# Optimization experiments

Measured on AMD Instinct MI355X. Metric: run time of the kernel, lower is better.

Reference implementation:

```python
import jax, jax.numpy as jnp
import numpy as np
from jax import lax

HUMAN_SIZE = 54
NUM_ACTIONS = 1
INPUT_SIZE = HUMAN_SIZE + NUM_ACTIONS  # 55, one_hot=True
RNN_SIZE = 1024
SOURCE_SEQ_LEN = 50
TARGET_SEQ_LEN = 25
BATCH = 1024


def setup_inputs() -> dict:
    key = jax.random.key(0)
    ks = jax.random.split(key, 8)
    s = 1.0 / np.sqrt(RNN_SIZE)
    return {
        "encoder_inputs": jax.random.normal(ks[0], (BATCH, SOURCE_SEQ_LEN, INPUT_SIZE), jnp.float32),
        "decoder_inputs": jax.random.normal(ks[1], (BATCH, TARGET_SEQ_LEN, INPUT_SIZE), jnp.float32),
        "W_ih": jax.random.uniform(ks[2], (3 * RNN_SIZE, INPUT_SIZE), jnp.float32, -s, s),
        "W_hh": jax.random.uniform(ks[3], (3 * RNN_SIZE, RNN_SIZE), jnp.float32, -s, s),
        "b_ih": jax.random.uniform(ks[4], (3 * RNN_SIZE,), jnp.float32, -s, s),
        "b_hh": jax.random.uniform(ks[5], (3 * RNN_SIZE,), jnp.float32, -s, s),
        "fc_w": jax.random.uniform(ks[6], (INPUT_SIZE, RNN_SIZE), jnp.float32, -s, s),
        "fc_b": jax.random.uniform(ks[7], (INPUT_SIZE,), jnp.float32, -s, s),
    }


def _gru_step(h, x, W_ih, W_hh, b_ih, b_hh):
    # torch.nn.GRUCell math
    gi = x @ W_ih.T + b_ih            # [B, 3H]
    gh = h @ W_hh.T + b_hh            # [B, 3H]
    i_r, i_z, i_n = jnp.split(gi, 3, axis=-1)
    h_r, h_z, h_n = jnp.split(gh, 3, axis=-1)
    r = jax.nn.sigmoid(i_r + h_r)
    z = jax.nn.sigmoid(i_z + h_z)
    n = jnp.tanh(i_n + r * h_n)
    return (1.0 - z) * n + z * h


def reference(encoder_inputs, decoder_inputs, W_ih, W_hh, b_ih, b_hh, fc_w, fc_b):
    B = encoder_inputs.shape[0]
    H = W_hh.shape[1]
    state0 = jnp.zeros((B, H), dtype=encoder_inputs.dtype)

    # Encoder: first source_seq_len-1 frames, time-major scan (dropout p=0 -> identity)
    enc_tm = jnp.swapaxes(encoder_inputs[:, : SOURCE_SEQ_LEN - 1], 0, 1)  # [S-1, B, In]

    def enc_step(h, x):
        return _gru_step(h, x, W_ih, W_hh, b_ih, b_hh), None

    state, _ = lax.scan(enc_step, state0, enc_tm)

    def dec_step(carry, _):
        h, inp = carry
        inp = lax.stop_gradient(inp)  # inp.detach()
        h = _gru_step(h, inp, W_ih, W_hh, b_ih, b_hh)
        out = inp + h @ fc_w.T + fc_b  # residual add
        return (h, out), out

    (_, _), outs = lax.scan(dec_step, (state, decoder_inputs[:, 0]), None, length=TARGET_SEQ_LEN)
    return jnp.swapaxes(outs, 0, 1)  # [B, T, In]
```

## Files before the change

### kernel.cpp

```cpp
#include <hip/hip_runtime.h>


typedef unsigned short ushort_t;
typedef __bf16 bf16x8 __attribute__((ext_vector_type(8)));
typedef float f32x4 __attribute__((ext_vector_type(4)));
typedef unsigned int u32x4 __attribute__((ext_vector_type(4)));

#define MFMA(a, b, c) __builtin_amdgcn_mfma_f32_16x16x32_bf16(a, b, c, 0, 0, 0)

static __device__ __forceinline__ ushort_t f2bf(float f) {
  union { float f; unsigned u; } x; x.f = f;
  unsigned r = x.u + 0x7fffu + ((x.u >> 16) & 1u);
  return (ushort_t)(r >> 16);
}
static __device__ __forceinline__ float sigmf(float x) { return 1.f / (1.f + __expf(-x)); }
static __device__ __forceinline__ float tanhf_(float x) { return 1.f - 2.f / (__expf(2.f * x) + 1.f); }

static __device__ __forceinline__ __amdgpu_buffer_rsrc_t mkrsrc(const void* p) {
  return __builtin_amdgcn_make_buffer_rsrc(const_cast<void*>(p), (short)0, -1, 0x00020000);
}
#if __has_builtin(__builtin_amdgcn_raw_buffer_load_b128)
static __device__ __forceinline__ bf16x8 ldb(__amdgpu_buffer_rsrc_t r, int voff) {
  u32x4 v = __builtin_amdgcn_raw_buffer_load_b128(r, voff, 0, 1);
  union { u32x4 u; bf16x8 b; } x; x.u = v; return x.b;
}
static __device__ __forceinline__ bf16x8 ldbc(__amdgpu_buffer_rsrc_t r, int voff) {
  u32x4 v = __builtin_amdgcn_raw_buffer_load_b128(r, voff, 0, 0);
  union { u32x4 u; bf16x8 b; } x; x.u = v; return x.b;
}
#else
static __device__ __forceinline__ bf16x8 ldb(__amdgpu_buffer_rsrc_t r, int voff) {
  union { unsigned u[4]; bf16x8 b; } x;
  x.u[0] = __builtin_amdgcn_raw_buffer_load_b32(r, voff, 0, 1);
  x.u[1] = __builtin_amdgcn_raw_buffer_load_b32(r, voff + 4, 0, 1);
  x.u[2] = __builtin_amdgcn_raw_buffer_load_b32(r, voff + 8, 0, 1);
  x.u[3] = __builtin_amdgcn_raw_buffer_load_b32(r, voff + 12, 0, 1);
  return x.b;
}
static __device__ __forceinline__ bf16x8 ldbc(__amdgpu_buffer_rsrc_t r, int voff) {
  union { unsigned u[4]; bf16x8 b; } x;
  x.u[0] = __builtin_amdgcn_raw_buffer_load_b32(r, voff, 0, 0);
  x.u[1] = __builtin_amdgcn_raw_buffer_load_b32(r, voff + 4, 0, 0);
  x.u[2] = __builtin_amdgcn_raw_buffer_load_b32(r, voff + 8, 0, 0);
  x.u[3] = __builtin_amdgcn_raw_buffer_load_b32(r, voff + 12, 0, 0);
  return x.b;
}
#endif

__global__ __launch_bounds__(512, 2)
void seq2seq_xcd(const float* __restrict__ enc, const float* __restrict__ dec,
                 const float* __restrict__ Wih, const float* __restrict__ Whh,
                 const float* __restrict__ b_ih, const float* __restrict__ b_hh,
                 const float* __restrict__ fcw, const float* __restrict__ fcb,
                 float* __restrict__ outp,
                 ushort_t* __restrict__ xg, ushort_t* __restrict__ hA,
                 ushort_t* __restrict__ innA, ushort_t* __restrict__ nG,
                 ushort_t* __restrict__ fcG, unsigned* cnt) {
  __shared__ ushort_t WrzL[65536];
  __shared__ ushort_t WiL[6144];
  __shared__ float scratchF[4096];
  __shared__ unsigned sgs;

  const int tid = threadIdx.x;
  const int w = tid >> 6, l = tid & 63;
  const int fr = l & 15, fq4 = l >> 4;

  if (tid == 0) {
    unsigned x;
    asm volatile("s_getreg_b32 %0, hwreg(HW_REG_XCC_ID, 0, 8)" : "=s"(x));
    x &= 7u;
    unsigned s = atomicAdd(&cnt[x * 64], 1u);
    sgs = (x << 8) | s;
  }
  __syncthreads();
  const int g = sgs >> 8, slot = sgs & 255;
  const bool isFC = (slot >= 24);

  unsigned* arrp = cnt + (8 + g) * 64;
  auto fcpp = [&](int td) { return cnt + (48 + g * 25 + td) * 64; };

  ushort_t* hbase = hA + (size_t)g * 262144;
  auto hb = [&](int i) { return hbase + (size_t)i * 131072; };
  ushort_t* xgg = xg + (size_t)g * 49 * 8192;
  auto inng = [&](int i) { return innA + (size_t)(g * 2 + i) * 8192; };
  ushort_t* nGp = nG + (size_t)(g * 32 + slot) * 32768;
  ushort_t* fcGg = fcG + (size_t)g * 65536;

  for (int i = tid; i < 65536; i += 512) {
    int j = i & 7, ln = (i >> 3) & 63, jf = (i >> 9) & 1, gt = (i >> 10) & 1, kt = i >> 11;
    int col = gt * 1024 + slot * 32 + jf * 16 + (ln & 15);
    int k = kt * 32 + (ln >> 4) * 8 + j;
    WrzL[i] = f2bf(Whh[(size_t)col * 1024 + k]);
  }
  for (int i = tid; i < 6144; i += 512) {
    int j = i & 7, ln = (i >> 3) & 63, jf = (i >> 9) & 1, rem = i >> 10;
    int gt = rem % 3, kt = rem / 3;
    int col = gt * 1024 + slot * 32 + jf * 16 + (ln & 15);
    int k = kt * 32 + (ln >> 4) * 8 + j;
    WiL[i] = (k < 55) ? f2bf(Wih[(size_t)col * 55 + k]) : (ushort_t)0;
  }
  for (int i = tid; i < 32768; i += 512) {
    int j = i & 7, ln = (i >> 3) & 63, jf = (i >> 9) & 1, kt = i >> 10;
    int col = 2048 + slot * 32 + jf * 16 + (ln & 15);
    int k = kt * 32 + (ln >> 4) * 8 + j;
    nGp[i] = f2bf(Whh[(size_t)col * 1024 + k]);
  }
#pragma unroll
  for (int rep = 0; rep < 2; ++rep) {
    int t = slot + rep * 32;
    if (t < 49) {
      ushort_t* xp = xgg + (size_t)t * 8192;
      for (int i = tid; i < 8192; i += 512) {
        int sub = i & 7, row = (i >> 3) & 127, kc = i >> 10;
        int c = kc * 8 + sub;
        xp[i] = (c < 55) ? f2bf(enc[((size_t)(g * 128 + row) * 50 + t) * 55 + c]) : (ushort_t)0;
      }
    }
  }
  if (slot < 4) {
    ushort_t* ip = inng(0);
    for (int i = slot * 2048 + tid; i < (slot + 1) * 2048; i += 512) {
      int sub = i & 7, row = (i >> 3) & 127, kc = i >> 10;
      int c = kc * 8 + sub;
      ip[i] = (c < 55) ? f2bf(dec[(size_t)(g * 128 + row) * 1375 + c]) : (ushort_t)0;
    }
  }
  if (isFC) {
    for (int i = (slot - 24) * 8192 + tid; i < (slot - 23) * 8192; i += 512) {
      int j = i & 7, ln = (i >> 3) & 63, jf = (i >> 9) & 3, kt = i >> 11;
      int c = jf * 16 + (ln & 15);
      int k = kt * 32 + (ln >> 4) * 8 + j;
      fcGg[i] = (c < 55) ? f2bf(fcw[(size_t)c * 1024 + k]) : (ushort_t)0;
    }
  }

  float brz[2], bzz[2], bin[2], bhn[2];
#pragma unroll
  for (int jf = 0; jf < 2; ++jf) {
    int col = slot * 32 + jf * 16 + fr;
    brz[jf] = b_ih[col] + b_hh[col];
    bzz[jf] = b_ih[1024 + col] + b_hh[1024 + col];
    bin[jf] = b_ih[2048 + col];
    bhn[jf] = b_hh[2048 + col];
  }
  const int Rfc = (slot - 24) * 16;
  const int jfF = w & 3;
  const int colF = jfF * 16 + fr;
  float fcbF = 0.f, inp[4] = {0.f, 0.f, 0.f, 0.f};
  if (isFC && w < 4) {
    fcbF = (colF < 55) ? fcb[colF] : 0.f;
#pragma unroll
    for (int v = 0; v < 4; ++v)
      inp[v] = (colF < 55) ? dec[(size_t)(g * 128 + Rfc + fq4 * 4 + v) * 1375 + colF] : 0.f;
  }
  f32x4 hreg[4];
#pragma unroll
  for (int i = 0; i < 4; ++i) hreg[i] = (f32x4){0.f, 0.f, 0.f, 0.f};

  auto arrive = [&](unsigned k) {
    (void)k;
    __syncthreads();
    if (tid == 0) atomicAdd(arrp, 1u);
  };
  auto wait_rel = [&](unsigned k) {
    if (tid == 0) {
      while (__hip_atomic_load(arrp, __ATOMIC_RELAXED, __HIP_MEMORY_SCOPE_AGENT) < 32u * k)
        __builtin_amdgcn_s_sleep(1);
    }
    __syncthreads();
  };
  auto fc_wait = [&](int td) {
    if (tid == 0) {
      while (__hip_atomic_load(fcpp(td), __ATOMIC_RELAXED, __HIP_MEMORY_SCOPE_AGENT) < 8u)
        __builtin_amdgcn_s_sleep(1);
    }
    __syncthreads();
  };

  f32x4 av[12], nx[4];

  auto xpart = [&](const ushort_t* xp) {
    __amdgpu_buffer_rsrc_t rx = mkrsrc(xp);
    const int R = w * 32;
#pragma unroll
    for (int kt = 0; kt < 2; ++kt) {
      bf16x8 a0 = ldb(rx, ((kt * 4 + fq4) * 128 + R + fr) * 16);
      bf16x8 a1 = ldb(rx, ((kt * 4 + fq4) * 128 + R + 16 + fr) * 16);
      const ushort_t* bl = WiL + kt * 3072 + l * 8;
#pragma unroll
      for (int jf = 0; jf < 2; ++jf) {
        bf16x8 br = *(const bf16x8*)(bl + jf * 512);
        bf16x8 bz = *(const bf16x8*)(bl + 1024 + jf * 512);
        bf16x8 bn = *(const bf16x8*)(bl + 2048 + jf * 512);
        av[jf] = MFMA(a0, br, av[jf]);
        av[2 + jf] = MFMA(a1, br, av[2 + jf]);
        av[4 + jf] = MFMA(a0, bz, av[4 + jf]);
        av[6 + jf] = MFMA(a1, bz, av[6 + jf]);
        nx[jf] = MFMA(a0, bn, nx[jf]);
        nx[2 + jf] = MFMA(a1, bn, nx[2 + jf]);
      }
    }
  };

  auto hpart = [&](const ushort_t* hbp) {
    __amdgpu_buffer_rsrc_t r = mkrsrc(hbp);
    __amdgpu_buffer_rsrc_t rn = mkrsrc(nGp);
    const int kh = w >> 2, R = (w & 3) * 32;
    bf16x8 A0[4], A1[4];
    bf16x8 NG[4][2];
#pragma unroll
    for (int i = 0; i < 4; ++i) {
      int kt = kh * 16 + i;
      A0[i] = ldb(r, ((kt * 4 + fq4) * 128 + R + fr) * 16);
      A1[i] = ldb(r, ((kt * 4 + fq4) * 128 + R + 16 + fr) * 16);
      NG[i][0] = ldbc(rn, kt * 2048 + l * 16);
      NG[i][1] = ldbc(rn, kt * 2048 + 1024 + l * 16);
    }
    const ushort_t* bl0 = WrzL + (kh * 16) * 2048 + l * 8;
    bf16x8 br0 = *(const bf16x8*)(bl0);
    bf16x8 br1 = *(const bf16x8*)(bl0 + 512);
    bf16x8 bz0 = *(const bf16x8*)(bl0 + 1024);
    bf16x8 bz1 = *(const bf16x8*)(bl0 + 1536);
#pragma unroll
    for (int i = 0; i < 16; ++i) {
      int kt = kh * 16 + i;
      bf16x8 a0 = A0[i & 3], a1 = A1[i & 3];
      bf16x8 n0 = NG[i & 3][0], n1 = NG[i & 3][1];
      bf16x8 cr0 = br0, cr1 = br1, cz0 = bz0, cz1 = bz1;
      if (i < 15) {
        const ushort_t* bln = WrzL + (kt + 1) * 2048 + l * 8;
        br0 = *(const bf16x8*)(bln);
        br1 = *(const bf16x8*)(bln + 512);
        bz0 = *(const bf16x8*)(bln + 1024);
        bz1 = *(const bf16x8*)(bln + 1536);
      }
      if (i < 12) {
        int kp = kt + 4;
        A0[i & 3] = ldb(r, ((kp * 4 + fq4) * 128 + R + fr) * 16);
        A1[i & 3] = ldb(r, ((kp * 4 + fq4) * 128 + R + 16 + fr) * 16);
        NG[i & 3][0] = ldbc(rn, kp * 2048 + l * 16);
        NG[i & 3][1] = ldbc(rn, kp * 2048 + 1024 + l * 16);
      }
      av[0] = MFMA(a0, cr0, av[0]);
      av[2] = MFMA(a1, cr0, av[2]);
      av[1] = MFMA(a0, cr1, av[1]);
      av[3] = MFMA(a1, cr1, av[3]);
      av[4] = MFMA(a0, cz0, av[4]);
      av[6] = MFMA(a1, cz0, av[6]);
      av[5] = MFMA(a0, cz1, av[5]);
      av[7] = MFMA(a1, cz1, av[7]);
      av[8] = MFMA(a0, n0, av[8]);
      av[10] = MFMA(a1, n0, av[10]);
      av[9] = MFMA(a0, n1, av[9]);
      av[11] = MFMA(a1, n1, av[11]);
    }
  };

  auto kreduce = [&]() {
#pragma unroll
    for (int rd = 0; rd < 3; ++rd) {
      if (w >= 4) {
        float* sp = scratchF + ((w - 4) * 64 + l) * 4;
#pragma unroll
        for (int r = 0; r < 4; ++r)
          *(f32x4*)(sp + r * 1024) = av[rd * 4 + r];
      }
      __syncthreads();
      if (w < 4) {
        const float* sp = scratchF + (w * 64 + l) * 4;
#pragma unroll
        for (int r = 0; r < 4; ++r)
          av[rd * 4 + r] += *(const f32x4*)(sp + r * 1024);
      }
      __syncthreads();
    }
  };

  auto fcdo = [&](const ushort_t* hbp, int td, bool wr, ushort_t* innW) {
    __amdgpu_buffer_rsrc_t r = mkrsrc(hbp);
    __amdgpu_buffer_rsrc_t rf = mkrsrc(fcGg);
    const int kh = w >> 2;
    f32x4 fa = (f32x4){0.f, 0.f, 0.f, 0.f};
    bf16x8 Af[4], Bf[4];
#pragma unroll
    for (int i = 0; i < 4; ++i) {
      int kt = kh * 16 + i;
      Af[i] = ldb(r, ((kt * 4 + fq4) * 128 + Rfc + fr) * 16);
      Bf[i] = ldbc(rf, (kt * 4 + jfF) * 1024 + l * 16);
    }
#pragma unroll
    for (int i = 0; i < 16; ++i) {
      int kt = kh * 16 + i;
      bf16x8 a = Af[i & 3], bb = Bf[i & 3];
      if (i < 12) {
        Af[i & 3] = ldb(r, (((kt + 4) * 4 + fq4) * 128 + Rfc + fr) * 16);
        Bf[i & 3] = ldbc(rf, ((kt + 4) * 4 + jfF) * 1024 + l * 16);
      }
      fa = MFMA(a, bb, fa);
    }
    if (w >= 4) *(f32x4*)(scratchF + ((w - 4) * 64 + l) * 4) = fa;
    __syncthreads();
    if (w < 4) {
      fa += *(const f32x4*)(scratchF + (w * 64 + l) * 4);
      const int kq = colF >> 3, sub = colF & 7;
#pragma unroll
      for (int v = 0; v < 4; ++v) {
        int row = Rfc + fq4 * 4 + v;
        float o = fa[v] + inp[v] + fcbF;
        inp[v] = o;
        if (wr) innW[(kq * 128 + row) * 8 + sub] = f2bf(o);
        if (colF < 55) outp[(size_t)(g * 128 + row) * 1375 + td * 55 + colF] = o;
      }
    }
    __syncthreads();
  };

  arrive(1);
  wait_rel(1);

  for (int t = 0; t < 74; ++t) {
#pragma unroll
    for (int i = 0; i < 12; ++i) av[i] = (f32x4){0.f, 0.f, 0.f, 0.f};
#pragma unroll
    for (int i = 0; i < 4; ++i) nx[i] = (f32x4){0.f, 0.f, 0.f, 0.f};

    if (t <= 49) {
      if (w < 4) xpart(t <= 48 ? xgg + (size_t)t * 8192 : inng(0));
    }
    if (t > 0) wait_rel(t + 1);
    if (t >= 50 && isFC) {
      fcdo(hb(t & 1), t - 50, true, inng((t - 49) & 1));
      if (tid == 0) atomicAdd(fcpp(t - 50), 1u);
    }
    if (t > 0) hpart(hb(t & 1));
    if (t >= 50) {
      fc_wait(t - 50);
      if (w < 4) xpart(inng((t - 49) & 1));
    }
    kreduce();
    if (w < 4) {
      ushort_t* hn = hb((t + 1) & 1);
#pragma unroll
      for (int mi = 0; mi < 2; ++mi)
#pragma unroll
        for (int jf = 0; jf < 2; ++jf) {
          f32x4 R_ = av[mi * 2 + jf], Z_ = av[4 + mi * 2 + jf];
          f32x4 NH = av[8 + mi * 2 + jf], NX = nx[mi * 2 + jf];
          const int kq = slot * 4 + jf * 2 + (fr >> 3), sub = fr & 7;
#pragma unroll
          for (int v = 0; v < 4; ++v) {
            float rr = sigmf(R_[v] + brz[jf]);
            float zz = sigmf(Z_[v] + bzz[jf]);
            float nn = tanhf_(NX[v] + bin[jf] + rr * (NH[v] + bhn[jf]));
            float h = (1.f - zz) * nn + zz * hreg[mi * 2 + jf][v];
            hreg[mi * 2 + jf][v] = h;
            int row = w * 32 + mi * 16 + fq4 * 4 + v;
            hn[(kq * 128 + row) * 8 + sub] = f2bf(h);
          }
        }
    }
    arrive(t + 2);
  }

  if (isFC) {
    wait_rel(75);
    fcdo(hb(0), 24, false, (ushort_t*)0);
  }
}

extern "C" void kernel_launch(void* const* d_in, const int* in_sizes, int n_in,
                              void* d_out, int out_size, void* d_ws, size_t ws_size,
                              hipStream_t stream) {
  const float* enc  = (const float*)d_in[0];
  const float* dec  = (const float*)d_in[1];
  const float* Wih  = (const float*)d_in[2];
  const float* Whh  = (const float*)d_in[3];
  const float* b_ih = (const float*)d_in[4];
  const float* b_hh = (const float*)d_in[5];
  const float* fcw  = (const float*)d_in[6];
  const float* fcb  = (const float*)d_in[7];
  float* out = (float*)d_out;

  char* ws = (char*)d_ws;
  unsigned* cnt  = (unsigned*)ws; ws += 65536;
  ushort_t* xg   = (ushort_t*)ws; ws += (size_t)8 * 49 * 8192 * 2;
  ushort_t* hA   = (ushort_t*)ws; ws += (size_t)8 * 2 * 131072 * 2;
  ushort_t* innA = (ushort_t*)ws; ws += (size_t)8 * 2 * 8192 * 2;
  ushort_t* nG   = (ushort_t*)ws; ws += (size_t)8 * 32 * 32768 * 2;
  ushort_t* fcG  = (ushort_t*)ws; ws += (size_t)8 * 65536 * 2;

  (void)hipMemsetAsync(cnt, 0, 65536, stream);
  seq2seq_xcd<<<256, 512, 0, stream>>>(
      enc, dec, Wih, Whh, b_ih, b_hh, fcw, fcb, out,
      xg, hA, innA, nG, fcG, cnt);
}
```

Baseline: 801.4 us.

## Split K-reduction and GRU epilogue across all eight waves instead of four

The cross-wave K reduction becomes a symmetric exchange. Each wave group writes the half of the tiles it does not own and reads back the half it does, so all eight waves finish reductions and the gate epilogue in parallel. The x-projection MFMAs are also split by row half across all waves. This halves per-wave epilogue transcendental and store work and the per-wave scratch traffic, at the cost of changing which wave owns which h rows.

Result: slower. 1.464 ms (+82.7%).

```diff
diff --git a/kernel.cpp b/kernel.cpp
--- a/kernel.cpp
+++ b/kernel.cpp
@@ -153,9 +153,9 @@
     for (int v = 0; v < 4; ++v)
       inp[v] = (colF < 55) ? dec[(size_t)(g * 128 + Rfc + fq4 * 4 + v) * 1375 + colF] : 0.f;
   }
-  f32x4 hreg[4];
-#pragma unroll
-  for (int i = 0; i < 4; ++i) hreg[i] = (f32x4){0.f, 0.f, 0.f, 0.f};
+  f32x4 hreg[2];
+#pragma unroll
+  for (int i = 0; i < 2; ++i) hreg[i] = (f32x4){0.f, 0.f, 0.f, 0.f};
 
   auto arrive = [&](unsigned k) {
     (void)k;
@@ -177,27 +177,28 @@
     __syncthreads();
   };
 
-  f32x4 av[12], nx[4];
+  f32x4 av[12], nxl[2];
 
   auto xpart = [&](const ushort_t* xp) {
     __amdgpu_buffer_rsrc_t rx = mkrsrc(xp);
-    const int R = w * 32;
+    const int R = (w & 3) * 32 + (w >> 2) * 16;
 #pragma unroll
     for (int kt = 0; kt < 2; ++kt) {
-      bf16x8 a0 = ldb(rx, ((kt * 4 + fq4) * 128 + R + fr) * 16);
-      bf16x8 a1 = ldb(rx, ((kt * 4 + fq4) * 128 + R + 16 + fr) * 16);
+      bf16x8 a = ldb(rx, ((kt * 4 + fq4) * 128 + R + fr) * 16);
       const ushort_t* bl = WiL + kt * 3072 + l * 8;
 #pragma unroll
       for (int jf = 0; jf < 2; ++jf) {
         bf16x8 br = *(const bf16x8*)(bl + jf * 512);
         bf16x8 bz = *(const bf16x8*)(bl + 1024 + jf * 512);
         bf16x8 bn = *(const bf16x8*)(bl + 2048 + jf * 512);
-        av[jf] = MFMA(a0, br, av[jf]);
-        av[2 + jf] = MFMA(a1, br, av[2 + jf]);
-        av[4 + jf] = MFMA(a0, bz, av[4 + jf]);
-        av[6 + jf] = MFMA(a1, bz, av[6 + jf]);
-        nx[jf] = MFMA(a0, bn, nx[jf]);
-        nx[2 + jf] = MFMA(a1, bn, nx[2 + jf]);
+        if (w < 4) {
+          av[jf] = MFMA(a, br, av[jf]);
+          av[4 + jf] = MFMA(a, bz, av[4 + jf]);
+        } else {
+          av[2 + jf] = MFMA(a, br, av[2 + jf]);
+          av[6 + jf] = MFMA(a, bz, av[6 + jf]);
+        }
+        nxl[jf] = MFMA(a, bn, nxl[jf]);
       }
     }
   };
@@ -256,24 +257,27 @@
     }
   };
 
-  auto kreduce = [&]() {
-#pragma unroll
-    for (int rd = 0; rd < 3; ++rd) {
-      if (w >= 4) {
-        float* sp = scratchF + ((w - 4) * 64 + l) * 4;
-#pragma unroll
-        for (int r = 0; r < 4; ++r)
-          *(f32x4*)(sp + r * 1024) = av[rd * 4 + r];
-      }
-      __syncthreads();
-      if (w < 4) {
-        const float* sp = scratchF + (w * 64 + l) * 4;
-#pragma unroll
-        for (int r = 0; r < 4; ++r)
-          av[rd * 4 + r] += *(const f32x4*)(sp + r * 1024);
-      }
-      __syncthreads();
-    }
+  auto kround = [&](f32x4& g0a, f32x4& g0b, f32x4& g1a, f32x4& g1b) {
+    if (w >= 4) {
+      float* sp = scratchF + ((w - 4) * 64 + l) * 4;
+      *(f32x4*)(sp) = g0a;
+      *(f32x4*)(sp + 1024) = g0b;
+    } else {
+      float* sp = scratchF + (w * 64 + l) * 4;
+      *(f32x4*)(sp + 2048) = g1a;
+      *(f32x4*)(sp + 3072) = g1b;
+    }
+    __syncthreads();
+    if (w < 4) {
+      const float* sp = scratchF + (w * 64 + l) * 4;
+      g0a += *(const f32x4*)(sp);
+      g0b += *(const f32x4*)(sp + 1024);
+    } else {
+      const float* sp = scratchF + ((w - 4) * 64 + l) * 4;
+      g1a += *(const f32x4*)(sp + 2048);
+      g1b += *(const f32x4*)(sp + 3072);
+    }
+    __syncthreads();
   };
 
   auto fcdo = [&](const ushort_t* hbp, int td, bool wr, ushort_t* innW) {
@@ -322,10 +326,10 @@
 #pragma unroll
     for (int i = 0; i < 12; ++i) av[i] = (f32x4){0.f, 0.f, 0.f, 0.f};
 #pragma unroll
-    for (int i = 0; i < 4; ++i) nx[i] = (f32x4){0.f, 0.f, 0.f, 0.f};
+    for (int i = 0; i < 2; ++i) nxl[i] = (f32x4){0.f, 0.f, 0.f, 0.f};
 
     if (t <= 49) {
-      if (w < 4) xpart(t <= 48 ? xgg + (size_t)t * 8192 : inng(0));
+      xpart(t <= 48 ? xgg + (size_t)t * 8192 : inng(0));
     }
     if (t > 0) wait_rel(t + 1);
     if (t >= 50 && isFC) {
@@ -335,29 +339,34 @@
     if (t > 0) hpart(hb(t & 1));
     if (t >= 50) {
       fc_wait(t - 50);
-      if (w < 4) xpart(inng((t - 49) & 1));
-    }
-    kreduce();
-    if (w < 4) {
+      xpart(inng((t - 49) & 1));
+    }
+    kround(av[0], av[1], av[2], av[3]);
+    kround(av[4], av[5], av[6], av[7]);
+    kround(av[8], av[9], av[10], av[11]);
+    {
       ushort_t* hn = hb((t + 1) & 1);
-#pragma unroll
-      for (int mi = 0; mi < 2; ++mi)
-#pragma unroll
-        for (int jf = 0; jf < 2; ++jf) {
-          f32x4 R_ = av[mi * 2 + jf], Z_ = av[4 + mi * 2 + jf];
-          f32x4 NH = av[8 + mi * 2 + jf], NX = nx[mi * 2 + jf];
-          const int kq = slot * 4 + jf * 2 + (fr >> 3), sub = fr & 7;
-#pragma unroll
-          for (int v = 0; v < 4; ++v) {
-            float rr = sigmf(R_[v] + brz[jf]);
-            float zz = sigmf(Z_[v] + bzz[jf]);
-            float nn = tanhf_(NX[v] + bin[jf] + rr * (NH[v] + bhn[jf]));
-            float h = (1.f - zz) * nn + zz * hreg[mi * 2 + jf][v];
-            hreg[mi * 2 + jf][v] = h;
-            int row = w * 32 + mi * 16 + fq4 * 4 + v;
-            hn[(kq * 128 + row) * 8 + sub] = f2bf(h);
-          }
+      const int Rbase = (w & 3) * 32 + (w >> 2) * 16;
+      auto epi = [&](f32x4 R_, f32x4 Z_, f32x4 NH, f32x4 NX, int jf, f32x4& hc) {
+        const int kq = slot * 4 + jf * 2 + (fr >> 3), sub = fr & 7;
+#pragma unroll
+        for (int v = 0; v < 4; ++v) {
+          float rr = sigmf(R_[v] + brz[jf]);
+          float zz = sigmf(Z_[v] + bzz[jf]);
+          float nn = tanhf_(NX[v] + bin[jf] + rr * (NH[v] + bhn[jf]));
+          float h = (1.f - zz) * nn + zz * hc[v];
+          hc[v] = h;
+          int row = Rbase + fq4 * 4 + v;
+          hn[(kq * 128 + row) * 8 + sub] = f2bf(h);
         }
+      };
+      if (w < 4) {
+        epi(av[0], av[4], av[8], nxl[0], 0, hreg[0]);
+        epi(av[1], av[5], av[9], nxl[1], 1, hreg[1]);
+      } else {
+        epi(av[2], av[6], av[10], nxl[0], 0, hreg[0]);
+        epi(av[3], av[7], av[11], nxl[1], 1, hreg[1]);
+      }
     }
     arrive(t + 2);
   }
```
